# Optimization experiments

Measured on AMD Instinct MI355X. Metric: run time of the kernel, lower is better.

## Reference

```python
import jax, jax.numpy as jnp
import numpy as np

B, INPUT_DIM, N = 8, 1, 4096
DIM, DEPTH, HEADS, DIM_HEAD = 512, 4, 8, 64
WINDOW = 128
NUM_CLASSES = 10
INNER = int(DIM * 4 * 2 / 3)  # 1365 (GEGLU FeedForward inner dim)
LN_EPS = 1e-5


def setup_inputs() -> dict:
    key = jax.random.key(0)
    ks = jax.random.split(key, 12)
    s = 0.02
    inner_qkv = HEADS * DIM_HEAD
    return {
        "x": jax.random.normal(ks[0], (B, INPUT_DIM, N), dtype=jnp.float32),
        "lin_emb_w": jax.random.normal(ks[1], (DIM, INPUT_DIM), dtype=jnp.float32) * s,
        "lin_emb_b": jnp.zeros((DIM,), dtype=jnp.float32),
        "qkv_w": jax.random.normal(ks[2], (DEPTH, 3 * inner_qkv, DIM), dtype=jnp.float32) * s,
        "out_w": jax.random.normal(ks[3], (DEPTH, DIM, inner_qkv), dtype=jnp.float32) * s,
        "ff_ln_g": jnp.ones((DEPTH, DIM), dtype=jnp.float32),
        "ff_ln_b": jnp.zeros((DEPTH, DIM), dtype=jnp.float32),
        "ff_w1": jax.random.normal(ks[4], (DEPTH, 2 * INNER, DIM), dtype=jnp.float32) * s,
        "ff_w2": jax.random.normal(ks[5], (DEPTH, DIM, INNER), dtype=jnp.float32) * s,
        "proj_w": jax.random.normal(ks[6], (NUM_CLASSES, DIM), dtype=jnp.float32) * s,
        "proj_b": jnp.zeros((NUM_CLASSES,), dtype=jnp.float32),
    }


def _layer_norm(x, g, b):
    mu = jnp.mean(x, axis=-1, keepdims=True)
    var = jnp.mean(jnp.square(x - mu), axis=-1, keepdims=True)
    return (x - mu) * jax.lax.rsqrt(var + LN_EPS) * g + b


def _local_attention(q, k, v, w):
    # q,k,v: (b, h, n, d). Non-causal sliding window: each window of size w
    # attends to windows [i-1, i, i+1] (look_backward=1, look_forward=1),
    # with out-of-range key positions masked (lucidrains LocalAttention,
    # autopad=True, exact_windowsize=False). n is a multiple of w here.
    b, h, n, d = q.shape
    nw = n // w
    scale = d ** -0.5
    qw = q.reshape(b, h, nw, w, d) * scale
    kw = k.reshape(b, h, nw, w, d)
    vw = v.reshape(b, h, nw, w, d)

    def look_around(t):  # (b,h,nw,w,d) -> (b,h,nw,3w,d)
        tp = jnp.pad(t, ((0, 0), (0, 0), (1, 1), (0, 0), (0, 0)))
        return jnp.concatenate([tp[:, :, i:i + nw] for i in range(3)], axis=3)

    k3 = look_around(kw)
    v3 = look_around(vw)

    # validity mask for boundary windows (fake keys from padding)
    win = jnp.arange(nw)
    kpos = (win[:, None] - 1) * w + jnp.arange(3 * w)[None, :]  # (nw, 3w)
    valid = (kpos >= 0) & (kpos < n)

    scores = jnp.einsum('bhnqd,bhnkd->bhnqk', qw, k3)  # (b,h,nw,w,3w)
    scores = jnp.where(valid[None, None, :, None, :], scores,
                       jnp.finfo(scores.dtype).min)
    attn = jax.nn.softmax(scores, axis=-1)
    out = jnp.einsum('bhnqk,bhnkd->bhnqd', attn, v3)
    return out.reshape(b, h, n, d)


def reference(x, lin_emb_w, lin_emb_b, qkv_w, out_w, ff_ln_g, ff_ln_b,
              ff_w1, ff_w2, proj_w, proj_b):
    b = x.shape[0]
    h = jnp.einsum('bdn,ed->bne', x, lin_emb_w) + lin_emb_b  # (b, n, dim)
    for l in range(DEPTH):
        # --- LocalMHA (no prenorm) + residual ---
        qkv = jnp.einsum('bnd,ed->bne', h, qkv_w[l])
        q, k, v = jnp.split(qkv, 3, axis=-1)
        def heads(t):
            return t.reshape(b, N, HEADS, DIM_HEAD).transpose(0, 2, 1, 3)
        o = _local_attention(heads(q), heads(k), heads(v), WINDOW)
        o = o.transpose(0, 2, 1, 3).reshape(b, N, HEADS * DIM_HEAD)
        h = jnp.einsum('bne,de->bnd', o, out_w[l]) + h
        # --- GEGLU FeedForward (prenorm inside) + residual ---
        y = _layer_norm(h, ff_ln_g[l], ff_ln_b[l])
        y = jnp.einsum('bnd,ed->bne', y, ff_w1[l])
        u, gate = jnp.split(y, 2, axis=-1)
        y = u * jax.nn.gelu(gate, approximate=False)
        h = h + jnp.einsum('bne,de->bnd', y, ff_w2[l])
    pooled = h.mean(axis=1)  # mean_pooling
    return pooled @ proj_w.T + proj_b
```

## Files before the change

kernel.cpp:

```cpp
#include <hip/hip_runtime.h>
#include <hip/hip_bf16.h>
#include <math.h>

typedef __attribute__((ext_vector_type(8))) short short8;
typedef __attribute__((ext_vector_type(4))) float f32x4;

#define MFMA16 __builtin_amdgcn_mfma_f32_16x16x32_bf16

__device__ __forceinline__ short f2bf(float f){
  unsigned u = __float_as_uint(f);
  u = (u + 0x7FFFu + ((u >> 16) & 1u)) >> 16;
  return (short)u;
}

__device__ __forceinline__ float gelu_phi(float g){
  float ax = fabsf(g) * 0.70710678118f;
  float t  = 1.f / (1.f + 0.3275911f * ax);
  float pp = ((((1.061405429f * t - 1.453152027f) * t + 1.421413741f) * t
               - 0.284496736f) * t + 0.254829592f) * t;
  float e  = 1.f - pp * __expf(-ax * ax);
  return 0.5f + copysignf(0.5f, g) * e;
}

__global__ void cast_bf16_kernel(const float* __restrict__ s, short* __restrict__ d, int n){
  int i = blockIdx.x * 256 + threadIdx.x;
  if (i < n) d[i] = f2bf(s[i]);
}

__global__ void w1p_kernel(const float* __restrict__ s, short* __restrict__ d){
  int i = blockIdx.x * 256 + threadIdx.x;
  int c  = i & 511;
  int rl = i >> 9;
  int r  = rl % 2816;
  int l  = rl / 2816;
  int g  = r >> 5, sfx = r & 31;
  int j  = g * 16 + (sfx & 15);
  float v = 0.f;
  if (j < 1365){
    int sr = (sfx < 16) ? j : 1365 + j;
    v = s[((size_t)l * 2730 + sr) * 512 + c];
  }
  d[i] = f2bf(v);
}

__global__ void w2p_kernel(const float* __restrict__ s, short* __restrict__ d){
  int i = blockIdx.x * 256 + threadIdx.x;
  int c = i % 1408;
  int r = i / 1408;
  float v = (c < 1365) ? s[(size_t)r * 1365 + c] : 0.f;
  d[i] = f2bf(v);
}

__global__ void embed_kernel(const float* __restrict__ x, const float* __restrict__ w,
                             const float* __restrict__ bias, float* __restrict__ hf,
                             short* __restrict__ hb){
  long i = (long)blockIdx.x * 256 + threadIdx.x;
  long row = i >> 9; int e = (int)(i & 511);
  float v = x[row] * w[e] + bias[e];
  hf[i] = v;
  hb[i] = f2bf(v);
}

template<int EPI>
__global__ __launch_bounds__(512, 2)
void gemm256(const short* __restrict__ A, const short* __restrict__ B, int K,
             float* __restrict__ Cres, short* __restrict__ Cbf, int ldcb)
{
  __shared__ short As[2][256][64];
  __shared__ short Bs[2][256][64];
  char* smA = (char*)As;
  char* smB = (char*)Bs;

  const int tid  = threadIdx.x;
  const int lane = tid & 63;
  const int w    = tid >> 6;
  const int wm   = w >> 2;
  const int wn   = w & 3;
  const int NT   = K >> 6;

  const int nwg = gridDim.x * gridDim.y;
  const int f   = blockIdx.y * gridDim.x + blockIdx.x;
  const int sw  = (f & 7) * (nwg >> 3) + (f >> 3);
  const long tm = (long)(sw / gridDim.x) * 256;
  const long tn = (long)(sw % gridDim.x) * 256;

  const int r0 = tid >> 3;
  const int c0 = (tid & 7) ^ (r0 & 7);
  const short* aS = A + (tm + r0) * (long)K + c0 * 8;
  const short* bS = B + (tn + r0) * (long)K + c0 * 8;
  const int ldsW0 = w * 1024;
  const int ldsW1 = 8192 + w * 1024;
  const long halfA = 128 * (long)K;

  auto stgA = [&](int dstoff, const short* srcp){
    __builtin_amdgcn_global_load_lds((const __attribute__((address_space(1))) void*)(srcp),
        (__attribute__((address_space(3))) void*)(smA + dstoff + ldsW0), 16, 0, 0);
    __builtin_amdgcn_global_load_lds((const __attribute__((address_space(1))) void*)(srcp + 64 * (long)K),
        (__attribute__((address_space(3))) void*)(smA + dstoff + ldsW1), 16, 0, 0);
  };
  auto stgB = [&](int dstoff, const short* srcp){
    __builtin_amdgcn_global_load_lds((const __attribute__((address_space(1))) void*)(srcp),
        (__attribute__((address_space(3))) void*)(smB + dstoff + ldsW0), 16, 0, 0);
    __builtin_amdgcn_global_load_lds((const __attribute__((address_space(1))) void*)(srcp + 64 * (long)K),
        (__attribute__((address_space(3))) void*)(smB + dstoff + ldsW1), 16, 0, 0);
  };

  f32x4 acc[8][4];
  #pragma unroll
  for (int i = 0; i < 8; i++)
    #pragma unroll
    for (int j = 0; j < 4; j++)
      acc[i][j] = (f32x4){0.f, 0.f, 0.f, 0.f};

  const int rb  = (lane & 15) * 128;
  const int ct0 = (((lane >> 4)    ) ^ (lane & 7)) * 16;
  const int ct1 = ((4 + (lane >> 4)) ^ (lane & 7)) * 16;

  stgB(0,             bS);
  stgA(0,             aS);
  stgA(16384,         aS + halfA);
  stgB(16384,         bS + halfA);
  if (NT > 1){
    stgB(32768,         bS + 64);
    stgA(32768,         aS + 64);
    stgA(32768 + 16384, aS + halfA + 64);
  }
  asm volatile("s_waitcnt vmcnt(6)" ::: "memory");
  __builtin_amdgcn_s_barrier();

  for (int t = 0; t < NT; ++t){
    const int cur = (t & 1) * 32768;
    const int nxt = 32768 - cur;
    const bool s1 = (t + 1 < NT), s2 = (t + 2 < NT);
    const long o1 = (long)(t + 1) * 64, o2 = (long)(t + 2) * 64;
    short8 a0[8], a1[8], bb[4][2];

    #pragma unroll
    for (int ni = 0; ni < 4; ni++){
      bb[ni][0] = *(const short8*)(smB + cur + wn * 8192 + ni * 2048 + rb + ct0);
      bb[ni][1] = *(const short8*)(smB + cur + wn * 8192 + ni * 2048 + rb + ct1);
    }
    #pragma unroll
    for (int mi = 0; mi < 8; mi++)
      a0[mi] = *(const short8*)(smA + cur + wm * 16384 + mi * 2048 + rb + ct0);
    if (s1) stgB(nxt + 16384, bS + halfA + o1);
    asm volatile("s_waitcnt lgkmcnt(0)" ::: "memory");
    __builtin_amdgcn_sched_barrier(0);
    __builtin_amdgcn_s_barrier();
    __builtin_amdgcn_s_setprio(1);
    #pragma unroll
    for (int mi = 0; mi < 8; mi++){
      acc[mi][0] = MFMA16(a0[mi], bb[0][0], acc[mi][0], 0, 0, 0);
      acc[mi][1] = MFMA16(a0[mi], bb[1][0], acc[mi][1], 0, 0, 0);
    }
    __builtin_amdgcn_s_setprio(0);
    __builtin_amdgcn_s_barrier();

    #pragma unroll
    for (int mi = 0; mi < 8; mi++)
      a1[mi] = *(const short8*)(smA + cur + wm * 16384 + mi * 2048 + rb + ct1);
    if (s2) stgB(cur, bS + o2);
    asm volatile("s_waitcnt lgkmcnt(0)" ::: "memory");
    __builtin_amdgcn_sched_barrier(0);
    __builtin_amdgcn_s_barrier();
    __builtin_amdgcn_s_setprio(1);
    #pragma unroll
    for (int mi = 0; mi < 8; mi++){
      acc[mi][2] = MFMA16(a0[mi], bb[2][0], acc[mi][2], 0, 0, 0);
      acc[mi][3] = MFMA16(a0[mi], bb[3][0], acc[mi][3], 0, 0, 0);
    }
    __builtin_amdgcn_s_setprio(0);
    __builtin_amdgcn_s_barrier();

    if (s2) stgA(cur, aS + o2);
    __builtin_amdgcn_s_barrier();
    __builtin_amdgcn_s_setprio(1);
    #pragma unroll
    for (int mi = 0; mi < 8; mi++){
      acc[mi][0] = MFMA16(a1[mi], bb[0][1], acc[mi][0], 0, 0, 0);
      acc[mi][1] = MFMA16(a1[mi], bb[1][1], acc[mi][1], 0, 0, 0);
    }
    __builtin_amdgcn_s_setprio(0);
    __builtin_amdgcn_s_barrier();

    if (s2) stgA(cur + 16384, aS + halfA + o2);
    if (t < NT - 2) asm volatile("s_waitcnt vmcnt(6)" ::: "memory");
    else            asm volatile("s_waitcnt vmcnt(0)" ::: "memory");
    __builtin_amdgcn_s_barrier();
    __builtin_amdgcn_s_setprio(1);
    #pragma unroll
    for (int mi = 0; mi < 8; mi++){
      acc[mi][2] = MFMA16(a1[mi], bb[2][1], acc[mi][2], 0, 0, 0);
      acc[mi][3] = MFMA16(a1[mi], bb[3][1], acc[mi][3], 0, 0, 0);
    }
    __builtin_amdgcn_s_setprio(0);
    __builtin_amdgcn_s_barrier();
  }

  #pragma unroll
  for (int mi = 0; mi < 8; mi++){
    if (EPI == 3){
      #pragma unroll
      for (int p = 0; p < 2; p++){
        #pragma unroll
        for (int v = 0; v < 4; v++){
          long row = tm + wm * 128 + mi * 16 + (lane >> 4) * 4 + v;
          long col = (tn >> 1) + wn * 32 + p * 16 + (lane & 15);
          float u = acc[mi][2 * p][v];
          float g = acc[mi][2 * p + 1][v];
          Cbf[row * ldcb + col] = f2bf(u * g * gelu_phi(g));
        }
      }
    } else {
      #pragma unroll
      for (int ni = 0; ni < 4; ni++){
        #pragma unroll
        for (int v = 0; v < 4; v++){
          long row = tm + wm * 128 + mi * 16 + (lane >> 4) * 4 + v;
          long col = tn + wn * 64 + ni * 16 + (lane & 15);
          float x = acc[mi][ni][v];
          if (EPI == 0){
            Cbf[row * ldcb + col] = f2bf(x);
          } else if (EPI == 1){
            Cres[row * 512 + col] = x + Cres[row * 512 + col];
          } else {
            float rr = x + Cres[row * 512 + col];
            Cres[row * 512 + col] = rr;
            Cbf[row * 512 + col] = f2bf(rr);
          }
        }
      }
    }
  }
}

__global__ __launch_bounds__(256, 2)
void attn_kernel(const short* __restrict__ qkv, short* __restrict__ o)
{
  __shared__ short Ks[128 * 64];
  __shared__ short Vt[64 * 136];
  __shared__ short Ps[4 * 32 * 128];
  const int win = blockIdx.x, hh = blockIdx.y, b = blockIdx.z;
  const int tid = threadIdx.x, lane = tid & 63, w = tid >> 6;
  const long qrow0 = (long)b * 4096 + (long)win * 128;

  short8 qf[2][2];
  #pragma unroll
  for (int i = 0; i < 2; i++)
    #pragma unroll
    for (int kk = 0; kk < 2; kk++)
      qf[i][kk] = *(const short8*)(qkv + (qrow0 + w * 32 + i * 16 + (lane & 15)) * 1536
                                   + hh * 64 + kk * 32 + (lane >> 4) * 8);

  f32x4 oacc[2][4];
  #pragma unroll
  for (int i = 0; i < 2; i++)
    #pragma unroll
    for (int j = 0; j < 4; j++)
      oacc[i][j] = (f32x4){0.f, 0.f, 0.f, 0.f};
  float rs[2][4];
  #pragma unroll
  for (int i = 0; i < 2; i++)
    #pragma unroll
    for (int v = 0; v < 4; v++)
      rs[i][v] = 0.f;

  const int row_s = tid >> 3, c_s = tid & 7;
  for (int cc = 0; cc < 3; cc++){
    int kw = win - 1 + cc;
    if (kw < 0 || kw >= 32) continue;
    const long krow0 = (long)b * 4096 + (long)kw * 128;
    __syncthreads();
    #pragma unroll
    for (int r = 0; r < 4; r++){
      int row = row_s + r * 32;
      const short* src = qkv + (krow0 + row) * 1536 + hh * 64;
      short8 kv = *(const short8*)(src + 512 + c_s * 8);
      *(short8*)((char*)Ks + ((row * 128 + c_s * 16) ^ ((row & 7) << 4))) = kv;
      short8 vv = *(const short8*)(src + 1024 + c_s * 8);
      #pragma unroll
      for (int e = 0; e < 8; e++) Vt[(c_s * 8 + e) * 136 + row] = vv[e];
    }
    __syncthreads();

    f32x4 sacc[2][8];
    #pragma unroll
    for (int i = 0; i < 2; i++)
      #pragma unroll
      for (int j = 0; j < 8; j++)
        sacc[i][j] = (f32x4){0.f, 0.f, 0.f, 0.f};
    #pragma unroll
    for (int kk = 0; kk < 2; kk++){
      short8 bbk[8];
      int ac = (kk * 32 + (lane >> 4) * 8) * 2;
      #pragma unroll
      for (int j = 0; j < 8; j++){
        int br = j * 16 + (lane & 15);
        bbk[j] = *(const short8*)((char*)Ks + ((br * 128 + ac) ^ ((br & 7) << 4)));
      }
      #pragma unroll
      for (int i = 0; i < 2; i++)
        #pragma unroll
        for (int j = 0; j < 8; j++)
          sacc[i][j] = MFMA16(qf[i][kk], bbk[j], sacc[i][j], 0, 0, 0);
    }

    short* myPs = Ps + w * 32 * 128;
    float psum[2][4];
    #pragma unroll
    for (int i = 0; i < 2; i++)
      #pragma unroll
      for (int v = 0; v < 4; v++)
        psum[i][v] = 0.f;
    #pragma unroll
    for (int i = 0; i < 2; i++)
      #pragma unroll
      for (int j = 0; j < 8; j++)
        #pragma unroll
        for (int v = 0; v < 4; v++){
          float p = expf(0.125f * sacc[i][j][v]);
          psum[i][v] += p;
          int prow = i * 16 + (lane >> 4) * 4 + v;
          int pcb  = (j * 16 + (lane & 15)) * 2;
          *(short*)((char*)myPs + ((prow * 256 + pcb) ^ ((prow & 7) << 4))) = f2bf(p);
        }
    #pragma unroll
    for (int i = 0; i < 2; i++)
      #pragma unroll
      for (int v = 0; v < 4; v++){
        float s = psum[i][v];
        s += __shfl_xor(s, 1); s += __shfl_xor(s, 2);
        s += __shfl_xor(s, 4); s += __shfl_xor(s, 8);
        rs[i][v] += s;
      }
    __syncthreads();

    #pragma unroll
    for (int kk = 0; kk < 4; kk++){
      short8 pa[2], vb[4];
      int kb = (kk * 32 + (lane >> 4) * 8) * 2;
      #pragma unroll
      for (int i = 0; i < 2; i++){
        int pr = i * 16 + (lane & 15);
        pa[i] = *(const short8*)((char*)myPs + ((pr * 256 + kb) ^ ((pr & 7) << 4)));
      }
      #pragma unroll
      for (int j = 0; j < 4; j++){
        int vr = j * 16 + (lane & 15);
        vb[j] = *(const short8*)((char*)Vt + (vr * 272 + kb));
      }
      #pragma unroll
      for (int i = 0; i < 2; i++)
        #pragma unroll
        for (int j = 0; j < 4; j++)
          oacc[i][j] = MFMA16(pa[i], vb[j], oacc[i][j], 0, 0, 0);
    }
  }

  #pragma unroll
  for (int i = 0; i < 2; i++)
    #pragma unroll
    for (int j = 0; j < 4; j++)
      #pragma unroll
      for (int v = 0; v < 4; v++){
        long row = qrow0 + w * 32 + i * 16 + (lane >> 4) * 4 + v;
        int col = hh * 64 + j * 16 + (lane & 15);
        o[row * 512 + col] = f2bf(oacc[i][j][v] / rs[i][v]);
      }
}

__global__ __launch_bounds__(256)
void ln_kernel(const float* __restrict__ h, const float* __restrict__ g,
               const float* __restrict__ be, short* __restrict__ y)
{
  long row = (long)blockIdx.x * 4 + (threadIdx.x >> 6);
  int lane = threadIdx.x & 63;
  const float* x = h + row * 512 + lane * 8;
  float4 a0 = *(const float4*)x;
  float4 a1 = *(const float4*)(x + 4);
  float v[8] = {a0.x, a0.y, a0.z, a0.w, a1.x, a1.y, a1.z, a1.w};
  float s = 0.f, sq = 0.f;
  #pragma unroll
  for (int j = 0; j < 8; j++){ s += v[j]; sq += v[j] * v[j]; }
  #pragma unroll
  for (int m = 1; m <= 32; m <<= 1){ s += __shfl_xor(s, m); sq += __shfl_xor(sq, m); }
  float mu = s * (1.f / 512.f);
  float var = sq * (1.f / 512.f) - mu * mu;
  float rstd = rsqrtf(var + 1e-5f);
  short* yo = y + row * 512 + lane * 8;
  #pragma unroll
  for (int j = 0; j < 8; j++){
    int c = lane * 8 + j;
    yo[j] = f2bf((v[j] - mu) * rstd * g[c] + be[c]);
  }
}

__global__ void pool_partial(const float* __restrict__ h, float* __restrict__ part){
  int b = blockIdx.x, ch = blockIdx.y, t = threadIdx.x;
  float s0 = 0.f, s1 = 0.f;
  const float* base = h + ((long)b * 4096 + ch * 128) * 512;
  for (int n = 0; n < 128; n++){
    s0 += base[(long)n * 512 + t];
    s1 += base[(long)n * 512 + t + 256];
  }
  part[((b * 32 + ch) * 512) + t] = s0;
  part[((b * 32 + ch) * 512) + t + 256] = s1;
}

__global__ void pool_proj(const float* __restrict__ part, const float* __restrict__ pw,
                          const float* __restrict__ pb, float* __restrict__ out){
  __shared__ float pooled[512];
  __shared__ float red[4];
  int b = blockIdx.x, t = threadIdx.x;
  int lane = t & 63, w = t >> 6;
  float s0 = 0.f, s1 = 0.f;
  for (int ch = 0; ch < 32; ch++){
    s0 += part[((b * 32 + ch) * 512) + t];
    s1 += part[((b * 32 + ch) * 512) + t + 256];
  }
  pooled[t] = s0 * (1.f / 4096.f);
  pooled[t + 256] = s1 * (1.f / 4096.f);
  __syncthreads();
  for (int cls = 0; cls < 10; cls++){
    float p = pooled[t] * pw[cls * 512 + t] + pooled[t + 256] * pw[cls * 512 + t + 256];
    p += __shfl_xor(p, 1); p += __shfl_xor(p, 2); p += __shfl_xor(p, 4);
    p += __shfl_xor(p, 8); p += __shfl_xor(p, 16); p += __shfl_xor(p, 32);
    if (lane == 0) red[w] = p;
    __syncthreads();
    if (t == 0) out[b * 10 + cls] = red[0] + red[1] + red[2] + red[3] + pb[cls];
    __syncthreads();
  }
}

extern "C" void kernel_launch(void* const* d_in, const int* in_sizes, int n_in,
                              void* d_out, int out_size, void* d_ws, size_t ws_size,
                              hipStream_t stream)
{
  const float* x      = (const float*)d_in[0];
  const float* lin_w  = (const float*)d_in[1];
  const float* lin_b  = (const float*)d_in[2];
  const float* qkvw_f = (const float*)d_in[3];
  const float* outw_f = (const float*)d_in[4];
  const float* lng    = (const float*)d_in[5];
  const float* lnb    = (const float*)d_in[6];
  const float* w1_f   = (const float*)d_in[7];
  const float* w2_f   = (const float*)d_in[8];
  const float* projw  = (const float*)d_in[9];
  const float* projb  = (const float*)d_in[10];
  float* out = (float*)d_out;

  char* ws = (char*)d_ws;
  float* hf32 = (float*)(ws);
  short* abuf = (short*)(ws + 67108864);
  short* qkvb = (short*)(ws + 100663296);
  short* gbuf = qkvb;
  short* obuf = (short*)(ws + 201326592);
  float* part = (float*)(ws + 234881024);
  short* wqkv = (short*)(ws + 235405312);
  short* wout = (short*)(ws + 247988224);
  short* w1p  = (short*)(ws + 250085376);
  short* w2p  = (short*)(ws + 261619712);

  cast_bf16_kernel<<<12288, 256, 0, stream>>>(qkvw_f, wqkv, 4 * 1536 * 512);
  cast_bf16_kernel<<<4096, 256, 0, stream>>>(outw_f, wout, 4 * 512 * 512);
  w1p_kernel<<<22528, 256, 0, stream>>>(w1_f, w1p);
  w2p_kernel<<<11264, 256, 0, stream>>>(w2_f, w2p);
  embed_kernel<<<65536, 256, 0, stream>>>(x, lin_w, lin_b, hf32, abuf);

  for (int l = 0; l < 4; l++){
    gemm256<0><<<dim3(6, 128), 512, 0, stream>>>(abuf, wqkv + (size_t)l * 1536 * 512, 512,
                                                 nullptr, qkvb, 1536);
    attn_kernel<<<dim3(32, 8, 8), 256, 0, stream>>>(qkvb, obuf);
    gemm256<1><<<dim3(2, 128), 512, 0, stream>>>(obuf, wout + (size_t)l * 512 * 512, 512,
                                                 hf32, nullptr, 0);
    ln_kernel<<<8192, 256, 0, stream>>>(hf32, lng + l * 512, lnb + l * 512, abuf);
    gemm256<3><<<dim3(11, 128), 512, 0, stream>>>(abuf, w1p + (size_t)l * 2816 * 512, 512,
                                                  nullptr, gbuf, 1408);
    gemm256<2><<<dim3(2, 128), 512, 0, stream>>>(gbuf, w2p + (size_t)l * 512 * 1408, 1408,
                                                 hf32, abuf, 512);
  }
  pool_partial<<<dim3(8, 32), 256, 0, stream>>>(hf32, part);
  pool_proj<<<8, 256, 0, stream>>>(part, projw, projb, out);
}
```

Measured before the change: 1.823 ms.

## Restructure GEMM main loop into four quarter-phases and vectorize embed kernel

The GEMM inner loop now splits each K-tile into four MFMA phases over halves of the M fragments. Only four A fragments and four B fragments are held in registers at a time, and the LDS reads and global-to-LDS prefetch issue points are reordered so that A for the next tile is fetched early and B two tiles ahead. This aims to cut register pressure and interleave loads with MFMAs better, at the cost of more barriers per tile and repeated B fragment loads. Separately, the embed kernel processes eight elements per thread with float4 and short8 vector loads and stores, launching eight times fewer blocks.

```diff
diff --git a/kernel.cpp b/kernel.cpp
--- a/kernel.cpp
+++ b/kernel.cpp
@@ -54,11 +54,21 @@
 __global__ void embed_kernel(const float* __restrict__ x, const float* __restrict__ w,
                              const float* __restrict__ bias, float* __restrict__ hf,
                              short* __restrict__ hb){
-  long i = (long)blockIdx.x * 256 + threadIdx.x;
+  long i = ((long)blockIdx.x * 256 + threadIdx.x) * 8;
   long row = i >> 9; int e = (int)(i & 511);
-  float v = x[row] * w[e] + bias[e];
-  hf[i] = v;
-  hb[i] = f2bf(v);
+  float xv = x[row];
+  float4 w0 = *(const float4*)(w + e),    w1 = *(const float4*)(w + e + 4);
+  float4 b0 = *(const float4*)(bias + e), b1 = *(const float4*)(bias + e + 4);
+  float4 o0, o1;
+  o0.x = xv * w0.x + b0.x; o0.y = xv * w0.y + b0.y;
+  o0.z = xv * w0.z + b0.z; o0.w = xv * w0.w + b0.w;
+  o1.x = xv * w1.x + b1.x; o1.y = xv * w1.y + b1.y;
+  o1.z = xv * w1.z + b1.z; o1.w = xv * w1.w + b1.w;
+  *(float4*)(hf + i) = o0; *(float4*)(hf + i + 4) = o1;
+  short8 hv;
+  hv[0] = f2bf(o0.x); hv[1] = f2bf(o0.y); hv[2] = f2bf(o0.z); hv[3] = f2bf(o0.w);
+  hv[4] = f2bf(o1.x); hv[5] = f2bf(o1.y); hv[6] = f2bf(o1.z); hv[7] = f2bf(o1.w);
+  *(short8*)(hb + i) = hv;
 }
 
 template<int EPI>
@@ -90,7 +100,7 @@
   const short* bS = B + (tn + r0) * (long)K + c0 * 8;
   const int ldsW0 = w * 1024;
   const int ldsW1 = 8192 + w * 1024;
-  const long halfA = 128 * (long)K;
+  const long halfR = 128 * (long)K;
 
   auto stgA = [&](int dstoff, const short* srcp){
     __builtin_amdgcn_global_load_lds((const __attribute__((address_space(1))) void*)(srcp),
@@ -112,20 +122,16 @@
     for (int j = 0; j < 4; j++)
       acc[i][j] = (f32x4){0.f, 0.f, 0.f, 0.f};
 
-  const int rb  = (lane & 15) * 128;
-  const int ct0 = (((lane >> 4)    ) ^ (lane & 7)) * 16;
-  const int ct1 = ((4 + (lane >> 4)) ^ (lane & 7)) * 16;
-
-  stgB(0,             bS);
-  stgA(0,             aS);
-  stgA(16384,         aS + halfA);
-  stgB(16384,         bS + halfA);
-  if (NT > 1){
-    stgB(32768,         bS + 64);
-    stgA(32768,         aS + 64);
-    stgA(32768 + 16384, aS + halfA + 64);
-  }
-  asm volatile("s_waitcnt vmcnt(6)" ::: "memory");
+  const int rb   = (lane & 15) * 128;
+  const int ct0  = (((lane >> 4)    ) ^ (lane & 7)) * 16;
+  const int ct1  = ((4 + (lane >> 4)) ^ (lane & 7)) * 16;
+  const int aoff = wm * 16384 + rb;
+  const int boff = wn * 8192 + rb;
+
+  stgB(0, bS);              stgB(16384, bS + halfR);
+  stgA(0, aS);              stgA(16384, aS + halfR);
+  stgB(32768, bS + 64);     stgB(32768 + 16384, bS + halfR + 64);
+  asm volatile("s_waitcnt vmcnt(4)" ::: "memory");
   __builtin_amdgcn_s_barrier();
 
   for (int t = 0; t < NT; ++t){
@@ -133,67 +139,77 @@
     const int nxt = 32768 - cur;
     const bool s1 = (t + 1 < NT), s2 = (t + 2 < NT);
     const long o1 = (long)(t + 1) * 64, o2 = (long)(t + 2) * 64;
-    short8 a0[8], a1[8], bb[4][2];
-
-    #pragma unroll
-    for (int ni = 0; ni < 4; ni++){
-      bb[ni][0] = *(const short8*)(smB + cur + wn * 8192 + ni * 2048 + rb + ct0);
-      bb[ni][1] = *(const short8*)(smB + cur + wn * 8192 + ni * 2048 + rb + ct1);
-    }
-    #pragma unroll
-    for (int mi = 0; mi < 8; mi++)
-      a0[mi] = *(const short8*)(smA + cur + wm * 16384 + mi * 2048 + rb + ct0);
-    if (s1) stgB(nxt + 16384, bS + halfA + o1);
+    short8 a[4], bb[4];
+
+    #pragma unroll
+    for (int ni = 0; ni < 4; ni++)
+      bb[ni] = *(const short8*)(smB + cur + boff + ni * 2048 + ct0);
+    #pragma unroll
+    for (int q = 0; q < 4; q++)
+      a[q] = *(const short8*)(smA + cur + aoff + q * 2048 + ct0);
+    if (s1) stgA(nxt, aS + o1);
+    __builtin_amdgcn_s_barrier();
     asm volatile("s_waitcnt lgkmcnt(0)" ::: "memory");
     __builtin_amdgcn_sched_barrier(0);
-    __builtin_amdgcn_s_barrier();
     __builtin_amdgcn_s_setprio(1);
     #pragma unroll
-    for (int mi = 0; mi < 8; mi++){
-      acc[mi][0] = MFMA16(a0[mi], bb[0][0], acc[mi][0], 0, 0, 0);
-      acc[mi][1] = MFMA16(a0[mi], bb[1][0], acc[mi][1], 0, 0, 0);
-    }
+    for (int q = 0; q < 4; q++)
+      #pragma unroll
+      for (int ni = 0; ni < 4; ni++)
+        acc[q][ni] = MFMA16(a[q], bb[ni], acc[q][ni], 0, 0, 0);
     __builtin_amdgcn_s_setprio(0);
     __builtin_amdgcn_s_barrier();
 
     #pragma unroll
-    for (int mi = 0; mi < 8; mi++)
-      a1[mi] = *(const short8*)(smA + cur + wm * 16384 + mi * 2048 + rb + ct1);
-    if (s2) stgB(cur, bS + o2);
+    for (int q = 0; q < 4; q++)
+      a[q] = *(const short8*)(smA + cur + aoff + (4 + q) * 2048 + ct0);
+    if (s1) stgA(nxt + 16384, aS + halfR + o1);
+    __builtin_amdgcn_s_barrier();
     asm volatile("s_waitcnt lgkmcnt(0)" ::: "memory");
     __builtin_amdgcn_sched_barrier(0);
-    __builtin_amdgcn_s_barrier();
     __builtin_amdgcn_s_setprio(1);
     #pragma unroll
-    for (int mi = 0; mi < 8; mi++){
-      acc[mi][2] = MFMA16(a0[mi], bb[2][0], acc[mi][2], 0, 0, 0);
-      acc[mi][3] = MFMA16(a0[mi], bb[3][0], acc[mi][3], 0, 0, 0);
-    }
+    for (int q = 0; q < 4; q++)
+      #pragma unroll
+      for (int ni = 0; ni < 4; ni++)
+        acc[4 + q][ni] = MFMA16(a[q], bb[ni], acc[4 + q][ni], 0, 0, 0);
     __builtin_amdgcn_s_setprio(0);
     __builtin_amdgcn_s_barrier();
 
-    if (s2) stgA(cur, aS + o2);
-    __builtin_amdgcn_s_barrier();
+    #pragma unroll
+    for (int ni = 0; ni < 4; ni++)
+      bb[ni] = *(const short8*)(smB + cur + boff + ni * 2048 + ct1);
+    #pragma unroll
+    for (int q = 0; q < 4; q++)
+      a[q] = *(const short8*)(smA + cur + aoff + q * 2048 + ct1);
+    __builtin_amdgcn_s_barrier();
+    asm volatile("s_waitcnt lgkmcnt(0)" ::: "memory");
+    __builtin_amdgcn_sched_barrier(0);
     __builtin_amdgcn_s_setprio(1);
     #pragma unroll
-    for (int mi = 0; mi < 8; mi++){
-      acc[mi][0] = MFMA16(a1[mi], bb[0][1], acc[mi][0], 0, 0, 0);
-      acc[mi][1] = MFMA16(a1[mi], bb[1][1], acc[mi][1], 0, 0, 0);
-    }
+    for (int q = 0; q < 4; q++)
+      #pragma unroll
+      for (int ni = 0; ni < 4; ni++)
+        acc[q][ni] = MFMA16(a[q], bb[ni], acc[q][ni], 0, 0, 0);
     __builtin_amdgcn_s_setprio(0);
     __builtin_amdgcn_s_barrier();
 
-    if (s2) stgA(cur + 16384, aS + halfA + o2);
-    if (t < NT - 2) asm volatile("s_waitcnt vmcnt(6)" ::: "memory");
-    else            asm volatile("s_waitcnt vmcnt(0)" ::: "memory");
-    __builtin_amdgcn_s_barrier();
+    #pragma unroll
+    for (int q = 0; q < 4; q++)
+      a[q] = *(const short8*)(smA + cur + aoff + (4 + q) * 2048 + ct1);
+    if (s2){ stgB(cur, bS + o2); stgB(cur + 16384, bS + halfR + o2); }
+    __builtin_amdgcn_s_barrier();
+    asm volatile("s_waitcnt lgkmcnt(0)" ::: "memory");
+    __builtin_amdgcn_sched_barrier(0);
     __builtin_amdgcn_s_setprio(1);
     #pragma unroll
-    for (int mi = 0; mi < 8; mi++){
-      acc[mi][2] = MFMA16(a1[mi], bb[2][1], acc[mi][2], 0, 0, 0);
-      acc[mi][3] = MFMA16(a1[mi], bb[3][1], acc[mi][3], 0, 0, 0);
-    }
+    for (int q = 0; q < 4; q++)
+      #pragma unroll
+      for (int ni = 0; ni < 4; ni++)
+        acc[4 + q][ni] = MFMA16(a[q], bb[ni], acc[4 + q][ni], 0, 0, 0);
     __builtin_amdgcn_s_setprio(0);
+    if (s2) asm volatile("s_waitcnt vmcnt(4)" ::: "memory");
+    else    asm volatile("s_waitcnt vmcnt(0)" ::: "memory");
     __builtin_amdgcn_s_barrier();
   }
 
@@ -465,7 +481,7 @@
   cast_bf16_kernel<<<4096, 256, 0, stream>>>(outw_f, wout, 4 * 512 * 512);
   w1p_kernel<<<22528, 256, 0, stream>>>(w1_f, w1p);
   w2p_kernel<<<11264, 256, 0, stream>>>(w2_f, w2p);
-  embed_kernel<<<65536, 256, 0, stream>>>(x, lin_w, lin_b, hf32, abuf);
+  embed_kernel<<<8192, 256, 0, stream>>>(x, lin_w, lin_b, hf32, abuf);
 
   for (int l = 0; l < 4; l++){
     gemm256<0><<<dim3(6, 128), 512, 0, stream>>>(abuf, wqkv + (size_t)l * 1536 * 512, 512,
```

Result: no change. 1.815 ms (-0.4%).
